# Performance work log

Measured on AMD Instinct MI355X. Metric: run time of the kernel, lower is better.

Reference implementation:

```python
import jax, jax.numpy as jnp
import numpy as np

B, T, E = 2, 2048, 1024
H = 16            # num_heads (global in source repo)
D = E // H        # head_len
LN_EPS = 1e-5


def setup_inputs() -> dict:
    key = jax.random.key(0)
    ks = jax.random.split(key, 12)
    s = lambda fan_in: 1.0 / np.sqrt(fan_in)
    return {
        "x":     jax.random.normal(ks[0], (B, T, E), jnp.float32),
        "ln1_g": jnp.ones((E,), jnp.float32),
        "ln1_b": jnp.zeros((E,), jnp.float32),
        "Wq":    jax.random.normal(ks[1], (E, E), jnp.float32) * s(E),
        "Wk":    jax.random.normal(ks[2], (E, E), jnp.float32) * s(E),
        "Wv":    jax.random.normal(ks[3], (E, E), jnp.float32) * s(E),
        "Wo":    jax.random.normal(ks[4], (E, E), jnp.float32) * s(E),
        "bo":    jnp.zeros((E,), jnp.float32),
        "ln2_g": jnp.ones((E,), jnp.float32),
        "ln2_b": jnp.zeros((E,), jnp.float32),
        "W1":    jax.random.normal(ks[5], (E, 4 * E), jnp.float32) * s(E),
        "b1":    jnp.zeros((4 * E,), jnp.float32),
        "W2":    jax.random.normal(ks[6], (4 * E, E), jnp.float32) * s(4 * E),
        "b2":    jnp.zeros((E,), jnp.float32),
    }


def _layernorm(x, g, b):
    mu = jnp.mean(x, axis=-1, keepdims=True)
    var = jnp.mean(jnp.square(x - mu), axis=-1, keepdims=True)
    return (x - mu) * jax.lax.rsqrt(var + LN_EPS) * g + b


def _attention(x, Wq, Wk, Wv, Wo, bo):
    b, t, e = x.shape
    q = (x @ Wq).reshape(b, t, H, D)
    k = (x @ Wk).reshape(b, t, H, D)
    v = (x @ Wv).reshape(b, t, H, D)
    scores = jnp.einsum("bqhd,bkhd->bhqk", q, k) / np.sqrt(D).astype(np.float32)
    causal = jnp.tril(jnp.ones((t, t), bool))
    scores = jnp.where(causal, scores, -jnp.inf)
    attn = jax.nn.softmax(scores, axis=-1)
    out = jnp.einsum("bhqk,bkhd->bqhd", attn, v).reshape(b, t, e)
    return out @ Wo + bo


def reference(x, ln1_g, ln1_b, Wq, Wk, Wv, Wo, bo, ln2_g, ln2_b, W1, b1, W2, b2):
    # pre-norm attention + residual (dropout=0 / eval mode)
    x = x + _attention(_layernorm(x, ln1_g, ln1_b), Wq, Wk, Wv, Wo, bo)
    # pre-norm MLP + residual
    h = _layernorm(x, ln2_g, ln2_b)
    h = jax.nn.relu(h @ W1 + b1) @ W2 + b2
    return x + h
```

## Files before the change

kernel.cpp:

```cpp
#include <hip/hip_runtime.h>
#include <cmath>
#include <cstdint>
#include <cstddef>

typedef __bf16 bf16_t;
typedef __bf16 bf16x8 __attribute__((ext_vector_type(8)));
typedef float  f32x4  __attribute__((ext_vector_type(4)));

#define B_   2
#define T_   2048
#define E_   1024
#define H_   16
#define D_   64
#define FF_  4096
#define NROW (B_ * T_)
#define QS_  (3 * E_)
#define NTI  (T_ / 64)

__global__ __launch_bounds__(256) void ln_kernel(
    const float* __restrict__ x, const float* __restrict__ g,
    const float* __restrict__ bta, bf16_t* __restrict__ out)
{
    int row = blockIdx.x;
    int tid = threadIdx.x;
    const float4* xr = (const float4*)(x + (size_t)row * E_);
    float4 v = xr[tid];
    float s  = v.x + v.y + v.z + v.w;
    float ss = v.x * v.x + v.y * v.y + v.z * v.z + v.w * v.w;
#pragma unroll
    for (int off = 32; off; off >>= 1) {
        s  += __shfl_xor(s, off);
        ss += __shfl_xor(ss, off);
    }
    __shared__ float red[8];
    int wave = tid >> 6, lane = tid & 63;
    if (lane == 0) { red[wave] = s; red[4 + wave] = ss; }
    __syncthreads();
    s  = red[0] + red[1] + red[2] + red[3];
    ss = red[4] + red[5] + red[6] + red[7];
    float mu   = s * (1.0f / E_);
    float var  = ss * (1.0f / E_) - mu * mu;
    float rstd = rsqrtf(var + 1e-5f);
    float4 gv = ((const float4*)g)[tid];
    float4 bv = ((const float4*)bta)[tid];
    union { bf16_t h[4]; ushort4 u; } pk;
    pk.h[0] = (bf16_t)((v.x - mu) * rstd * gv.x + bv.x);
    pk.h[1] = (bf16_t)((v.y - mu) * rstd * gv.y + bv.y);
    pk.h[2] = (bf16_t)((v.z - mu) * rstd * gv.z + bv.z);
    pk.h[3] = (bf16_t)((v.w - mu) * rstd * gv.w + bv.w);
    ((ushort4*)(out + (size_t)row * E_))[tid] = pk.u;
}

__global__ __launch_bounds__(256) void ln_reduce2(
    const float* __restrict__ p, const float* __restrict__ bias,
    const float* __restrict__ resid, float* __restrict__ x1,
    const float* __restrict__ g, const float* __restrict__ bta,
    bf16_t* __restrict__ out)
{
    int row = blockIdx.x;
    int tid = threadIdx.x;
    size_t off = (size_t)row * E_;
    float4 v0 = ((const float4*)(p + off))[tid];
    float4 v1 = ((const float4*)(p + (size_t)NROW * E_ + off))[tid];
    float4 bb = ((const float4*)bias)[tid];
    float4 rr = ((const float4*)(resid + off))[tid];
    float4 v;
    v.x = v0.x + v1.x + bb.x + rr.x;
    v.y = v0.y + v1.y + bb.y + rr.y;
    v.z = v0.z + v1.z + bb.z + rr.z;
    v.w = v0.w + v1.w + bb.w + rr.w;
    ((float4*)(x1 + off))[tid] = v;
    float s  = v.x + v.y + v.z + v.w;
    float ss = v.x * v.x + v.y * v.y + v.z * v.z + v.w * v.w;
#pragma unroll
    for (int o = 32; o; o >>= 1) {
        s  += __shfl_xor(s, o);
        ss += __shfl_xor(ss, o);
    }
    __shared__ float red[8];
    int wave = tid >> 6, lane = tid & 63;
    if (lane == 0) { red[wave] = s; red[4 + wave] = ss; }
    __syncthreads();
    s  = red[0] + red[1] + red[2] + red[3];
    ss = red[4] + red[5] + red[6] + red[7];
    float mu   = s * (1.0f / E_);
    float var  = ss * (1.0f / E_) - mu * mu;
    float rstd = rsqrtf(var + 1e-5f);
    float4 gv = ((const float4*)g)[tid];
    float4 bv = ((const float4*)bta)[tid];
    union { bf16_t h[4]; ushort4 u; } pk;
    pk.h[0] = (bf16_t)((v.x - mu) * rstd * gv.x + bv.x);
    pk.h[1] = (bf16_t)((v.y - mu) * rstd * gv.y + bv.y);
    pk.h[2] = (bf16_t)((v.z - mu) * rstd * gv.z + bv.z);
    pk.h[3] = (bf16_t)((v.w - mu) * rstd * gv.w + bv.w);
    ((ushort4*)(out + off))[tid] = pk.u;
}

__global__ __launch_bounds__(256) void add_reduce4(
    const float* __restrict__ p, const float* __restrict__ bias,
    const float* __restrict__ resid, float* __restrict__ out)
{
    int row = blockIdx.x;
    int tid = threadIdx.x;
    size_t off = (size_t)row * E_;
    const size_t MN = (size_t)NROW * E_;
    float4 v0 = ((const float4*)(p + off))[tid];
    float4 v1 = ((const float4*)(p + MN + off))[tid];
    float4 v2 = ((const float4*)(p + 2 * MN + off))[tid];
    float4 v3 = ((const float4*)(p + 3 * MN + off))[tid];
    float4 bb = ((const float4*)bias)[tid];
    float4 rr = ((const float4*)(resid + off))[tid];
    float4 v;
    v.x = (v0.x + v1.x) + (v2.x + v3.x) + bb.x + rr.x;
    v.y = (v0.y + v1.y) + (v2.y + v3.y) + bb.y + rr.y;
    v.z = (v0.z + v1.z) + (v2.z + v3.z) + bb.z + rr.z;
    v.w = (v0.w + v1.w) + (v2.w + v3.w) + bb.w + rr.w;
    ((float4*)(out + off))[tid] = v;
}

__global__ __launch_bounds__(256) void transpose_all(
    const float* __restrict__ Wq, const float* __restrict__ Wk,
    const float* __restrict__ Wv, const float* __restrict__ Wo,
    const float* __restrict__ W1, const float* __restrict__ W2,
    bf16_t* __restrict__ wqkv, bf16_t* __restrict__ wot,
    bf16_t* __restrict__ w1t, bf16_t* __restrict__ w2t)
{
    int l = blockIdx.x;
    const float* W; bf16_t* Wt; int K, N, bx, by;
    if (l < 4096) {
        int seg = l >> 10, r = l & 1023;
        K = E_; N = E_; bx = r & 31; by = r >> 5;
        if      (seg == 0) { W = Wq; Wt = wqkv; }
        else if (seg == 1) { W = Wk; Wt = wqkv + (size_t)E_ * E_; }
        else if (seg == 2) { W = Wv; Wt = wqkv + (size_t)2 * E_ * E_; }
        else               { W = Wo; Wt = wot; }
    } else if (l < 8192) {
        int r = l - 4096; K = E_; N = FF_; bx = r & 127; by = r >> 7;
        W = W1; Wt = w1t;
    } else {
        int r = l - 8192; K = FF_; N = E_; bx = r & 31; by = r >> 5;
        W = W2; Wt = w2t;
    }
    __shared__ float t[32][33];
    int n0 = bx * 32, k0 = by * 32;
    int tx = threadIdx.x & 31, ty = threadIdx.x >> 5;
#pragma unroll
    for (int i = 0; i < 4; ++i)
        t[ty + i * 8][tx] = W[(size_t)(k0 + ty + i * 8) * N + n0 + tx];
    __syncthreads();
#pragma unroll
    for (int i = 0; i < 4; ++i)
        Wt[(size_t)(n0 + ty + i * 8) * K + k0 + tx] = (bf16_t)t[tx][ty + i * 8];
}

__device__ __forceinline__ void gload16(const bf16_t* g, bf16_t* l)
{
    __builtin_amdgcn_global_load_lds(
        (const __attribute__((address_space(1))) void*)g,
        (__attribute__((address_space(3))) void*)l, 16, 0, 0);
}

#define BM 128
#define BN 128
#define BK 64

__global__ __launch_bounds__(256) void gemm_bt(
    const bf16_t* __restrict__ A, const bf16_t* __restrict__ Bt,
    const float* __restrict__ bias, const float* __restrict__ resid,
    void* __restrict__ Cout, bf16_t* __restrict__ vt_out,
    int M, int N, int K, int lda, int ldb,
    int has_bias, int do_relu, int has_resid, int out_bf16)
{
    __shared__ __attribute__((aligned(16))) bf16_t As[BM * BK];
    __shared__ __attribute__((aligned(16))) bf16_t Bs[BN * BK];
    int tid  = threadIdx.x;
    int lane = tid & 63, wave = tid >> 6;
    int m0 = blockIdx.x * BM, n0 = blockIdx.y * BN;
    int wm = (wave & 1) * 64, wn = (wave >> 1) * 64;
    int koff = blockIdx.z * K;
    f32x4 acc[4][4];
#pragma unroll
    for (int i = 0; i < 4; ++i)
#pragma unroll
        for (int j = 0; j < 4; ++j) acc[i][j] = (f32x4){0.f, 0.f, 0.f, 0.f};

    const int ml = lane & 15;
    const int g  = lane >> 4;
    const int swl = ml & 7;

    int r8 = lane >> 3;
    int scw = ((lane & 7) ^ r8) * 8;
    const bf16_t* Ag = A  + (size_t)(m0 + wave * 32 + r8) * lda + koff + scw;
    const bf16_t* Bg = Bt + (size_t)(n0 + wave * 32 + r8) * ldb + koff + scw;
    bf16_t* Asw = &As[wave * 32 * BK];
    bf16_t* Bsw = &Bs[wave * 32 * BK];
    int niter = K / BK;

#pragma unroll
    for (int j = 0; j < 4; ++j) {
        gload16(Ag + (size_t)j * 8 * lda, Asw + j * 8 * BK);
        gload16(Bg + (size_t)j * 8 * ldb, Bsw + j * 8 * BK);
    }

    const char* Ac = (const char*)As;
    const char* Bc = (const char*)Bs;
    for (int it = 0; it < niter; ++it) {
        __syncthreads();
#pragma unroll
        for (int ks = 0; ks < 2; ++ks) {
            int swc = (((ks << 2) + g) ^ swl) << 4;
            bf16x8 af[4], bfr[4];
#pragma unroll
            for (int mi = 0; mi < 4; ++mi)
                af[mi] = *(const bf16x8*)(Ac + (wm + mi * 16 + ml) * 128 + swc);
#pragma unroll
            for (int ni = 0; ni < 4; ++ni)
                bfr[ni] = *(const bf16x8*)(Bc + (wn + ni * 16 + ml) * 128 + swc);
#pragma unroll
            for (int mi = 0; mi < 4; ++mi)
#pragma unroll
                for (int ni = 0; ni < 4; ++ni)
                    acc[mi][ni] = __builtin_amdgcn_mfma_f32_16x16x32_bf16(
                        af[mi], bfr[ni], acc[mi][ni], 0, 0, 0);
        }
        if (it + 1 < niter) {
            __syncthreads();
            int k0 = (it + 1) * BK;
#pragma unroll
            for (int j = 0; j < 4; ++j) {
                gload16(Ag + k0 + (size_t)j * 8 * lda, Asw + j * 8 * BK);
                gload16(Bg + k0 + (size_t)j * 8 * ldb, Bsw + j * 8 * BK);
            }
        }
    }

    int r4 = (lane >> 4) * 4;
    if (gridDim.z > 1) {
        float* P = (float*)Cout + (size_t)blockIdx.z * M * N;
#pragma unroll
        for (int mi = 0; mi < 4; ++mi)
#pragma unroll
            for (int ni = 0; ni < 4; ++ni) {
                int col = n0 + wn + ni * 16 + ml;
#pragma unroll
                for (int r = 0; r < 4; ++r) {
                    int row = m0 + wm + mi * 16 + r4 + r;
                    P[(size_t)row * N + col] = acc[mi][ni][r];
                }
            }
        return;
    }
#pragma unroll
    for (int mi = 0; mi < 4; ++mi) {
#pragma unroll
        for (int ni = 0; ni < 4; ++ni) {
            int col = n0 + wn + ni * 16 + ml;
            float bval = has_bias ? bias[col] : 0.0f;
#pragma unroll
            for (int r = 0; r < 4; ++r) {
                int row = m0 + wm + mi * 16 + r4 + r;
                float v = acc[mi][ni][r] + bval;
                if (do_relu)   v = fmaxf(v, 0.0f);
                if (has_resid) v += resid[(size_t)row * N + col];
                if (out_bf16)
                    ((bf16_t*)Cout)[(size_t)row * N + col] = (bf16_t)v;
                else
                    ((float*)Cout)[(size_t)row * N + col] = v;
            }
        }
    }
}

__device__ __forceinline__ void g256_stage_half(
    const bf16_t* gbase, int ldg, bf16_t* lhalf, int wave, int lane)
{
    int r = lane >> 3, c = lane & 7;
    int sc = (c ^ r) * 8;
#pragma unroll
    for (int j = 0; j < 2; ++j) {
        const bf16_t* src = gbase + (size_t)(wave * 8 + j * 64 + r) * ldg + sc;
        bf16_t* dst = lhalf + (wave * 8 + j * 64) * 64;
        __builtin_amdgcn_global_load_lds(
            (const __attribute__((address_space(1))) void*)src,
            (__attribute__((address_space(3))) void*)dst, 16, 0, 0);
    }
}

__device__ __forceinline__ bf16x8 g256_frag(const bf16_t* half, int row, int kb)
{
    return *(const bf16x8*)((const char*)half + row * 128 + (kb ^ ((row & 7) << 4)));
}

template<int FP, bool DO_BFR>
__device__ __forceinline__ void g256_reads(
    const bf16_t* Ahx, const bf16_t* Bhx,
    bf16x8 (&af)[2][2], bf16x8 (&bfr)[4][2],
    int ml, int kq16, int brow0)
{
    if (DO_BFR) {
#pragma unroll
        for (int ni = 0; ni < 4; ++ni) {
            bfr[ni][0] = g256_frag(Bhx, brow0 + ni * 16 + ml, kq16);
            bfr[ni][1] = g256_frag(Bhx, brow0 + ni * 16 + ml, 64 + kq16);
        }
    }
#pragma unroll
    for (int i = 0; i < 2; ++i) {
        af[i][0] = g256_frag(Ahx, (2 * FP + i) * 16 + ml, kq16);
        af[i][1] = g256_frag(Ahx, (2 * FP + i) * 16 + ml, 64 + kq16);
    }
}

template<int FP>
__device__ __forceinline__ void g256_mfma(
    const bf16x8 (&af)[2][2], const bf16x8 (&bfr)[4][2], f32x4 (&acc)[8][4])
{
    __builtin_amdgcn_s_setprio(1);
#pragma unroll
    for (int i = 0; i < 2; ++i)
#pragma unroll
        for (int ni = 0; ni < 4; ++ni)
#pragma unroll
            for (int ks = 0; ks < 2; ++ks)
                acc[2 * FP + i][ni] = __builtin_amdgcn_mfma_f32_16x16x32_bf16(
                    af[i][ks], bfr[ni][ks], acc[2 * FP + i][ni], 0, 0, 0);
    __builtin_amdgcn_s_setprio(0);
}

#define AHALF(t, h) (ldsr + ((((t) & 1) * 4 + (h)) * (128 * 64)))
#define BHALF(t, h) (ldsr + ((((t) & 1) * 4 + 2 + (h)) * (128 * 64)))
#define STG_A(t, h) g256_stage_half(Ab + (size_t)((h) * 128) * lda + (t) * 64, lda, AHALF(t, h), wave, lane)
#define STG_B(t, h) g256_stage_half(Bb + (size_t)((h) * 128) * ldb + (t) * 64, ldb, BHALF(t, h), wave, lane)
#define SBAR() __builtin_amdgcn_s_barrier()

__global__ __launch_bounds__(512, 2) void gemm256(
    const bf16_t* __restrict__ A, const bf16_t* __restrict__ Bt,
    const float* __restrict__ bias,
    void* __restrict__ Cout, bf16_t* __restrict__ vt_out,
    int M, int N, int K, int lda, int ldb,
    int has_bias, int do_relu, int split)
{
    extern __shared__ __attribute__((aligned(16))) bf16_t ldsr[];
    int tid = threadIdx.x, lane = tid & 63, wave = tid >> 6;
    int m0 = blockIdx.x * 256, n0 = blockIdx.y * 256;
    int koff = blockIdx.z * K;
    int ml = lane & 15, kq16 = (lane >> 4) * 16, r4 = (lane >> 4) * 4;
    int wr = (wave >> 2) * 128, wc = (wave & 3) * 64;
    int brow0 = (wave & 1) * 64;

    const bf16_t* Ab = A  + (size_t)m0 * lda + koff;
    const bf16_t* Bb = Bt + (size_t)n0 * ldb + koff;

    const bf16_t* A0 = AHALF(0, wave >> 2);
    const bf16_t* A1 = AHALF(1, wave >> 2);
    const bf16_t* B0 = BHALF(0, (wave & 3) >> 1);
    const bf16_t* B1 = BHALF(1, (wave & 3) >> 1);

    f32x4 acc[8][4];
#pragma unroll
    for (int i = 0; i < 8; ++i)
#pragma unroll
        for (int j = 0; j < 4; ++j) acc[i][j] = (f32x4){0.f, 0.f, 0.f, 0.f};
    bf16x8 bfr[4][2];

    STG_B(0, 0); STG_B(0, 1);
    STG_A(0, 0); STG_A(0, 1);
    STG_B(1, 0); STG_B(1, 1);
    asm volatile("s_waitcnt vmcnt(4)" ::: "memory");
    SBAR();

    int NIT2 = K / 128;
    for (int it = 0; it < NIT2; ++it) {
        bool last = (it == NIT2 - 1);
        int t1 = 2 * it + 1, t2 = 2 * it + 2, t3 = 2 * it + 3;
        bf16x8 af[2][2];

        g256_reads<0, true>(A0, B0, af, bfr, ml, kq16, brow0);
        STG_A(t1, 0);
        SBAR();
        g256_mfma<0>(af, bfr, acc);
        SBAR();

        g256_reads<1, false>(A0, B0, af, bfr, ml, kq16, brow0);
        STG_A(t1, 1);
        SBAR();
        g256_mfma<1>(af, bfr, acc);
        SBAR();

        g256_reads<2, false>(A0, B0, af, bfr, ml, kq16, brow0);
        if (!last) STG_B(t2, 0);
        SBAR();
        g256_mfma<2>(af, bfr, acc);
        SBAR();

        g256_reads<3, false>(A0, B0, af, bfr, ml, kq16, brow0);
        if (!last) STG_B(t2, 1);
        SBAR();
        g256_mfma<3>(af, bfr, acc);
        if (last) asm volatile("s_waitcnt vmcnt(0)" ::: "memory");
        else      asm volatile("s_waitcnt vmcnt(4)" ::: "memory");
        SBAR();

        g256_reads<0, true>(A1, B1, af, bfr, ml, kq16, brow0);
        if (!last) STG_A(t2, 0);
        SBAR();
        g256_mfma<0>(af, bfr, acc);
        SBAR();

        g256_reads<1, false>(A1, B1, af, bfr, ml, kq16, brow0);
        if (!last) STG_A(t2, 1);
        SBAR();
        g256_mfma<1>(af, bfr, acc);
        SBAR();

        g256_reads<2, false>(A1, B1, af, bfr, ml, kq16, brow0);
        if (!last) STG_B(t3, 0);
        SBAR();
        g256_mfma<2>(af, bfr, acc);
        SBAR();

        g256_reads<3, false>(A1, B1, af, bfr, ml, kq16, brow0);
        if (!last) STG_B(t3, 1);
        SBAR();
        g256_mfma<3>(af, bfr, acc);
        if (!last) asm volatile("s_waitcnt vmcnt(4)" ::: "memory");
        SBAR();
    }

    if (split > 1) {
        float* P = (float*)Cout + (size_t)blockIdx.z * M * N;
#pragma unroll
        for (int mi = 0; mi < 8; ++mi)
#pragma unroll
            for (int ni = 0; ni < 4; ++ni) {
                int col = n0 + wc + ni * 16 + ml;
#pragma unroll
                for (int r = 0; r < 4; ++r) {
                    int row = m0 + wr + mi * 16 + r4 + r;
                    P[(size_t)row * N + col] = acc[mi][ni][r];
                }
            }
        return;
    }
    if (vt_out && n0 >= 2 * E_) {
#pragma unroll
        for (int mi = 0; mi < 8; ++mi)
#pragma unroll
            for (int ni = 0; ni < 4; ++ni) {
                int vcol = n0 + wc + ni * 16 + ml - 2 * E_;
                int h = vcol >> 6, d = vcol & 63;
                int row0 = m0 + wr + mi * 16 + r4;
                int b = row0 >> 11, t = row0 & (T_ - 1);
                union { bf16_t h4[4]; uint2 u; } pk;
#pragma unroll
                for (int r = 0; r < 4; ++r) pk.h4[r] = (bf16_t)acc[mi][ni][r];
                *(uint2*)&vt_out[((size_t)(b * H_ + h) * D_ + d) * T_ + t] = pk.u;
            }
        return;
    }
#pragma unroll
    for (int mi = 0; mi < 8; ++mi) {
#pragma unroll
        for (int ni = 0; ni < 4; ++ni) {
            int col = n0 + wc + ni * 16 + ml;
            float bval = has_bias ? bias[col] : 0.0f;
#pragma unroll
            for (int r = 0; r < 4; ++r) {
                int row = m0 + wr + mi * 16 + r4 + r;
                float v = acc[mi][ni][r] + bval;
                if (do_relu) v = fmaxf(v, 0.0f);
                ((bf16_t*)Cout)[(size_t)row * N + col] = (bf16_t)v;
            }
        }
    }
}

#define PSTR 72
#define QSCL 0.1803368801111204f

__device__ __forceinline__ float exp2_hw(float x)
{
    float r;
    asm("v_exp_f32 %0, %1" : "=v"(r) : "v"(x));
    return r;
}

struct TileState {
    f32x4 acc[4];
    float l1;
};

__device__ __forceinline__ void attn_stage8(
    const bf16_t* kb, const bf16_t* vb,
    bf16_t* ksl, bf16_t* vsl, int wave, int lane)
{
    int r = lane >> 3;
    int sc = ((lane & 7) ^ r) * 8;
    int rb = wave * 8;
    gload16(kb + (size_t)(rb + r) * QS_ + sc, ksl + rb * 64);
    gload16(vb + (size_t)(rb + r) * T_  + sc, vsl + rb * 64);
}

__device__ __forceinline__ void tile_update(
    const bf16x8 kf[2][4], const bf16x8 vf[2][4], const bf16x8 qf[2],
    TileState& st, bf16_t* PsW, int ml, int r4, int kq8,
    bool diag, int ch, int qrow)
{
    f32x4 s[4];
    __builtin_amdgcn_s_setprio(1);
#pragma unroll
    for (int nt = 0; nt < 4; ++nt) {
        s[nt] = (f32x4){0.f, 0.f, 0.f, 0.f};
#pragma unroll
        for (int ks = 0; ks < 2; ++ks)
            s[nt] = __builtin_amdgcn_mfma_f32_16x16x32_bf16(kf[ks][nt], qf[ks], s[nt], 0, 0, 0);
    }
    __builtin_amdgcn_s_setprio(0);
    if (diag) {
#pragma unroll
        for (int nt = 0; nt < 4; ++nt)
#pragma unroll
            for (int r = 0; r < 4; ++r)
                if (ch * 64 + nt * 16 + r4 + r > qrow) s[nt][r] = -INFINITY;
    }
    float sum = 0.f;
#pragma unroll
    for (int nt = 0; nt < 4; ++nt)
#pragma unroll
        for (int r = 0; r < 4; ++r) {
            float p = exp2_hw(s[nt][r]);
            s[nt][r] = p;
            sum += p;
        }
    st.l1 += sum;

#pragma unroll
    for (int nt = 0; nt < 4; ++nt) {
        union { bf16_t h[4]; uint2 u; } pk;
#pragma unroll
        for (int r = 0; r < 4; ++r) pk.h[r] = (bf16_t)s[nt][r];
        *(uint2*)&PsW[ml * PSTR + nt * 16 + r4] = pk.u;
    }
    __builtin_amdgcn_s_setprio(1);
#pragma unroll
    for (int ks = 0; ks < 2; ++ks) {
        bf16x8 pf = *(const bf16x8*)&PsW[ml * PSTR + ks * 32 + kq8];
#pragma unroll
        for (int dt = 0; dt < 4; ++dt)
            st.acc[dt] = __builtin_amdgcn_mfma_f32_16x16x32_bf16(vf[ks][dt], pf, st.acc[dt], 0, 0, 0);
    }
    __builtin_amdgcn_s_setprio(0);
}

__global__ __launch_bounds__(512, 4) void attn_mfma(
    const bf16_t* __restrict__ Qp, const bf16_t* __restrict__ Kp,
    const bf16_t* __restrict__ Vt, bf16_t* __restrict__ O)
{
    __shared__ __attribute__((aligned(16))) bf16_t Ks[2][64 * 64];
    __shared__ __attribute__((aligned(16))) bf16_t Vts[2][64 * 64];
    __shared__ __attribute__((aligned(16))) bf16_t Ps[8][16 * PSTR];

    int tid = threadIdx.x, lane = tid & 63, wave = tid >> 6;
    int ml  = lane & 15;
    int kq8 = (lane >> 4) * 8;
    int g   = lane >> 4;
    int r4  = (lane >> 4) * 4;
    int swl = ml & 7;
    int bh = blockIdx.y, b = bh >> 4, h = bh & 15;
    size_t qk_base = (size_t)b * T_ * QS_ + h * D_;
    size_t vt_base = (size_t)bh * D_ * T_;
    size_t o_base  = (size_t)b * T_ * E_ + h * D_;

    int lo = blockIdx.x, hi = NTI - 1 - blockIdx.x;
    int half = wave >> 2, w4 = wave & 3;
    int qtile = half ? lo : hi;
    int qw = qtile * 64 + w4 * 16;

    bf16x8 qf[2];
#pragma unroll
    for (int ks = 0; ks < 2; ++ks) {
        bf16x8 a = *(const bf16x8*)&Qp[qk_base + (size_t)(qw + ml) * QS_ + ks * 32 + kq8];
#pragma unroll
        for (int j = 0; j < 8; ++j)
            a[j] = (bf16_t)((float)a[j] * QSCL);
        qf[ks] = a;
    }

    TileState st;
#pragma unroll
    for (int dt = 0; dt < 4; ++dt)
        st.acc[dt] = (f32x4){0.f, 0.f, 0.f, 0.f};
    st.l1 = 0.f;

    int nch = hi + 1;

    attn_stage8(Kp + qk_base, Vt + vt_base, Ks[0], Vts[0], wave, lane);

    for (int ch = 0; ch < nch; ++ch) {
        int cur = ch & 1, nxt = cur ^ 1;
        __syncthreads();

        if (ch + 1 < nch)
            attn_stage8(Kp + qk_base + (size_t)((ch + 1) * 64) * QS_,
                        Vt + vt_base + (ch + 1) * 64,
                        Ks[nxt], Vts[nxt], wave, lane);

        if (ch <= qtile) {
            bf16x8 kf[2][4], vf[2][4];
            const char* kc = (const char*)Ks[cur];
            const char* vc = (const char*)Vts[cur];
#pragma unroll
            for (int ks = 0; ks < 2; ++ks) {
                int swc = (((ks << 2) + g) ^ swl) << 4;
#pragma unroll
                for (int nt = 0; nt < 4; ++nt) {
                    int off = (nt * 16 + ml) * 128 + swc;
                    kf[ks][nt] = *(const bf16x8*)(kc + off);
                    vf[ks][nt] = *(const bf16x8*)(vc + off);
                }
            }
            tile_update(kf, vf, qf, st, Ps[wave], ml, r4, kq8,
                        ch == qtile, ch, qw + ml);
        }
    }

    {
        float l1 = st.l1;
        l1 += __shfl_xor(l1, 16);
        l1 += __shfl_xor(l1, 32);
        float inv = 1.0f / l1;
        bf16_t* PsW = Ps[wave];
#pragma unroll
        for (int dt = 0; dt < 4; ++dt) {
            union { bf16_t h[4]; uint2 u; } pk;
#pragma unroll
            for (int r = 0; r < 4; ++r) pk.h[r] = (bf16_t)(st.acc[dt][r] * inv);
            *(uint2*)&PsW[ml * PSTR + dt * 16 + r4] = pk.u;
        }
        int row = lane >> 2, seg = (lane & 3) * 16;
        bf16x8 o0 = *(const bf16x8*)&PsW[row * PSTR + seg];
        bf16x8 o1 = *(const bf16x8*)&PsW[row * PSTR + seg + 8];
        size_t gp = o_base + (size_t)(qw + row) * E_ + seg;
        *(bf16x8*)&O[gp]     = o0;
        *(bf16x8*)&O[gp + 8] = o1;
    }
}

extern "C" void kernel_launch(void* const* d_in, const int* in_sizes, int n_in,
                              void* d_out, int out_size, void* d_ws, size_t ws_size,
                              hipStream_t stream)
{
    const float* x    = (const float*)d_in[0];
    const float* ln1g = (const float*)d_in[1];
    const float* ln1b = (const float*)d_in[2];
    const float* Wq   = (const float*)d_in[3];
    const float* Wk   = (const float*)d_in[4];
    const float* Wv   = (const float*)d_in[5];
    const float* Wo   = (const float*)d_in[6];
    const float* bo   = (const float*)d_in[7];
    const float* ln2g = (const float*)d_in[8];
    const float* ln2b = (const float*)d_in[9];
    const float* W1   = (const float*)d_in[10];
    const float* b1   = (const float*)d_in[11];
    const float* W2   = (const float*)d_in[12];
    const float* b2   = (const float*)d_in[13];

    char* ws = (char*)d_ws;
    const size_t MB = 1024ull * 1024ull;
    bf16_t* w2t     = (bf16_t*)(ws + 0 * MB);
    float*  x1      = (float*)(ws + 8 * MB);
    float*  part_wo = (float*)(ws + 24 * MB);
    bf16_t* h1      = (bf16_t*)(ws + 24 * MB);
    bf16_t* w1t     = (bf16_t*)(ws + 56 * MB);
    bf16_t* xn      = (bf16_t*)(ws + 64 * MB);
    bf16_t* hb      = (bf16_t*)(ws + 64 * MB);
    bf16_t* wqkv    = (bf16_t*)(ws + 72 * MB);
    bf16_t* wot     = (bf16_t*)(ws + 78 * MB);
    bf16_t* QKV     = (bf16_t*)(ws + 80 * MB);
    bf16_t* Vtb     = (bf16_t*)(ws + 104 * MB);
    bf16_t* att     = (bf16_t*)(ws + 112 * MB);
    float*  part4   = (float*)(ws + 56 * MB);

    dim3 blk(256), blk5(512);
    const size_t LDS256 = 8 * 128 * 64 * sizeof(bf16_t);

    transpose_all<<<dim3(12288), blk, 0, stream>>>(
        Wq, Wk, Wv, Wo, W1, W2, wqkv, wot, w1t, w2t);

    ln_kernel<<<dim3(NROW), blk, 0, stream>>>(x, ln1g, ln1b, xn);

    gemm256<<<dim3(NROW / 256, QS_ / 256, 1), blk5, LDS256, stream>>>(
        xn, wqkv, nullptr, QKV, Vtb, NROW, QS_, E_, E_, E_, 0, 0, 1);

    attn_mfma<<<dim3(NTI / 2, B_ * H_), dim3(512), 0, stream>>>(
        QKV, QKV + E_, Vtb, att);

    gemm_bt<<<dim3(NROW / BM, E_ / BN, 2), blk, 0, stream>>>(
        att, wot, nullptr, nullptr, part_wo, nullptr, NROW, E_, E_ / 2, E_, E_, 0, 0, 0, 0);
    ln_reduce2<<<dim3(NROW), blk, 0, stream>>>(
        part_wo, bo, x, x1, ln2g, ln2b, hb);

    gemm256<<<dim3(NROW / 256, FF_ / 256, 1), blk5, LDS256, stream>>>(
        hb, w1t, b1, h1, nullptr, NROW, FF_, E_, E_, E_, 1, 1, 1);

    gemm256<<<dim3(NROW / 256, E_ / 256, 4), blk5, LDS256, stream>>>(
        h1, w2t, nullptr, part4, nullptr, NROW, E_, FF_ / 4, FF_, FF_, 0, 0, 4);
    add_reduce4<<<dim3(NROW), blk, 0, stream>>>(
        part4, b2, x1, (float*)d_out);
}
```

Before: 319.7 us.

## Store split-K partials in fp16 and remap GEMM workgroups for locality

Split-K partial sums from the Wo and W2 GEMMs are now written and read as fp16 instead of fp32, which halves the traffic of the partial buffers and the reduce kernels. Both GEMM kernels also remap the linear workgroup id with a stride-8 interleave, so consecutive launched blocks land on different chiplets/XCDs to improve cache locality. The fp16 partials can lose precision or overflow on large values.

```diff
diff --git a/kernel.cpp b/kernel.cpp
--- a/kernel.cpp
+++ b/kernel.cpp
@@ -4,6 +4,7 @@
 #include <cstddef>
 
 typedef __bf16 bf16_t;
+typedef _Float16 f16_t;
 typedef __bf16 bf16x8 __attribute__((ext_vector_type(8)));
 typedef float  f32x4  __attribute__((ext_vector_type(4)));
 
@@ -16,6 +17,13 @@
 #define NROW (B_ * T_)
 #define QS_  (3 * E_)
 #define NTI  (T_ / 64)
+
+__device__ __forceinline__ float4 ld4h(const f16_t* p)
+{
+    union { ushort4 u; f16_t h[4]; } c;
+    c.u = *(const ushort4*)p;
+    return make_float4((float)c.h[0], (float)c.h[1], (float)c.h[2], (float)c.h[3]);
+}
 
 __global__ __launch_bounds__(256) void ln_kernel(
     const float* __restrict__ x, const float* __restrict__ g,
@@ -52,7 +60,7 @@
 }
 
 __global__ __launch_bounds__(256) void ln_reduce2(
-    const float* __restrict__ p, const float* __restrict__ bias,
+    const f16_t* __restrict__ p, const float* __restrict__ bias,
     const float* __restrict__ resid, float* __restrict__ x1,
     const float* __restrict__ g, const float* __restrict__ bta,
     bf16_t* __restrict__ out)
@@ -60,8 +68,8 @@
     int row = blockIdx.x;
     int tid = threadIdx.x;
     size_t off = (size_t)row * E_;
-    float4 v0 = ((const float4*)(p + off))[tid];
-    float4 v1 = ((const float4*)(p + (size_t)NROW * E_ + off))[tid];
+    float4 v0 = ld4h(p + off + tid * 4);
+    float4 v1 = ld4h(p + (size_t)NROW * E_ + off + tid * 4);
     float4 bb = ((const float4*)bias)[tid];
     float4 rr = ((const float4*)(resid + off))[tid];
     float4 v;
@@ -97,25 +105,25 @@
 }
 
 __global__ __launch_bounds__(256) void add_reduce4(
-    const float* __restrict__ p, const float* __restrict__ bias,
+    const f16_t* __restrict__ p, const float* __restrict__ bias,
     const float* __restrict__ resid, float* __restrict__ out)
 {
     int row = blockIdx.x;
     int tid = threadIdx.x;
-    size_t off = (size_t)row * E_;
+    size_t off = (size_t)row * E_ + tid * 4;
     const size_t MN = (size_t)NROW * E_;
-    float4 v0 = ((const float4*)(p + off))[tid];
-    float4 v1 = ((const float4*)(p + MN + off))[tid];
-    float4 v2 = ((const float4*)(p + 2 * MN + off))[tid];
-    float4 v3 = ((const float4*)(p + 3 * MN + off))[tid];
+    float4 v0 = ld4h(p + off);
+    float4 v1 = ld4h(p + MN + off);
+    float4 v2 = ld4h(p + 2 * MN + off);
+    float4 v3 = ld4h(p + 3 * MN + off);
     float4 bb = ((const float4*)bias)[tid];
-    float4 rr = ((const float4*)(resid + off))[tid];
+    float4 rr = ((const float4*)(resid + (size_t)row * E_))[tid];
     float4 v;
     v.x = (v0.x + v1.x) + (v2.x + v3.x) + bb.x + rr.x;
     v.y = (v0.y + v1.y) + (v2.y + v3.y) + bb.y + rr.y;
     v.z = (v0.z + v1.z) + (v2.z + v3.z) + bb.z + rr.z;
     v.w = (v0.w + v1.w) + (v2.w + v3.w) + bb.w + rr.w;
-    ((float4*)(out + off))[tid] = v;
+    ((float4*)(out + (size_t)row * E_))[tid] = v;
 }
 
 __global__ __launch_bounds__(256) void transpose_all(
@@ -175,7 +183,10 @@
     __shared__ __attribute__((aligned(16))) bf16_t Bs[BN * BK];
     int tid  = threadIdx.x;
     int lane = tid & 63, wave = tid >> 6;
-    int m0 = blockIdx.x * BM, n0 = blockIdx.y * BN;
+    int gx = gridDim.x, nwg = gx * gridDim.y;
+    int orig = blockIdx.y * gx + blockIdx.x;
+    int wg = (orig & 7) * (nwg >> 3) + (orig >> 3);
+    int m0 = (wg % gx) * BM, n0 = (wg / gx) * BN;
     int wm = (wave & 1) * 64, wn = (wave >> 1) * 64;
     int koff = blockIdx.z * K;
     f32x4 acc[4][4];
@@ -236,7 +247,7 @@
 
     int r4 = (lane >> 4) * 4;
     if (gridDim.z > 1) {
-        float* P = (float*)Cout + (size_t)blockIdx.z * M * N;
+        f16_t* P = (f16_t*)Cout + (size_t)blockIdx.z * M * N;
 #pragma unroll
         for (int mi = 0; mi < 4; ++mi)
 #pragma unroll
@@ -245,7 +256,7 @@
 #pragma unroll
                 for (int r = 0; r < 4; ++r) {
                     int row = m0 + wm + mi * 16 + r4 + r;
-                    P[(size_t)row * N + col] = acc[mi][ni][r];
+                    P[(size_t)row * N + col] = (f16_t)acc[mi][ni][r];
                 }
             }
         return;
@@ -342,7 +353,10 @@
 {
     extern __shared__ __attribute__((aligned(16))) bf16_t ldsr[];
     int tid = threadIdx.x, lane = tid & 63, wave = tid >> 6;
-    int m0 = blockIdx.x * 256, n0 = blockIdx.y * 256;
+    int gx = gridDim.x, nwg = gx * gridDim.y;
+    int orig = blockIdx.y * gx + blockIdx.x;
+    int wg = (orig & 7) * (nwg >> 3) + (orig >> 3);
+    int m0 = (wg % gx) * 256, n0 = (wg / gx) * 256;
     int koff = blockIdx.z * K;
     int ml = lane & 15, kq16 = (lane >> 4) * 16, r4 = (lane >> 4) * 4;
     int wr = (wave >> 2) * 128, wc = (wave & 3) * 64;
@@ -428,7 +442,7 @@
     }
 
     if (split > 1) {
-        float* P = (float*)Cout + (size_t)blockIdx.z * M * N;
+        f16_t* P = (f16_t*)Cout + (size_t)blockIdx.z * M * N;
 #pragma unroll
         for (int mi = 0; mi < 8; ++mi)
 #pragma unroll
@@ -437,7 +451,7 @@
 #pragma unroll
                 for (int r = 0; r < 4; ++r) {
                     int row = m0 + wr + mi * 16 + r4 + r;
-                    P[(size_t)row * N + col] = acc[mi][ni][r];
+                    P[(size_t)row * N + col] = (f16_t)acc[mi][ni][r];
                 }
             }
         return;
@@ -669,7 +683,7 @@
     const size_t MB = 1024ull * 1024ull;
     bf16_t* w2t     = (bf16_t*)(ws + 0 * MB);
     float*  x1      = (float*)(ws + 8 * MB);
-    float*  part_wo = (float*)(ws + 24 * MB);
+    f16_t*  part_wo = (f16_t*)(ws + 24 * MB);
     bf16_t* h1      = (bf16_t*)(ws + 24 * MB);
     bf16_t* w1t     = (bf16_t*)(ws + 56 * MB);
     bf16_t* xn      = (bf16_t*)(ws + 64 * MB);
@@ -679,7 +693,7 @@
     bf16_t* QKV     = (bf16_t*)(ws + 80 * MB);
     bf16_t* Vtb     = (bf16_t*)(ws + 104 * MB);
     bf16_t* att     = (bf16_t*)(ws + 112 * MB);
-    float*  part4   = (float*)(ws + 56 * MB);
+    f16_t*  part4   = (f16_t*)(ws + 56 * MB);
 
     dim3 blk(256), blk5(512);
     const size_t LDS256 = 8 * 128 * 64 * sizeof(bf16_t);
```

Result: faster. 309.5 us (-3.2%).
